# Optimization experiments

Measured on AMD Instinct MI355X. Metric: run time of the kernel, lower is better.

Reference implementation:

```python
import jax, jax.numpy as jnp
import numpy as np

IMAGE_H, IMAGE_W = 256, 704
Z, Y, X = 128, 8, 128
BOUNDS = (-50.0, 50.0, -5.0, 5.0, -50.0, 50.0)
CENTROID = (0.0, 1.0, 0.0)
EPS_MEAN = 1e-6
EPS_DEPTH = 1e-4


def _compose_rt(R, t):
    M = jnp.zeros(R.shape[:-2] + (4, 4), R.dtype)
    M = M.at[..., :3, :3].set(R)
    M = M.at[..., :3, 3].set(t)
    M = M.at[..., 3, 3].set(1.0)
    return M


def _safe_inverse(M):
    R = M[..., :3, :3]
    t = M[..., :3, 3]
    Rt = jnp.swapaxes(R, -1, -2)
    return _compose_rt(Rt, -jnp.einsum('...ij,...j->...i', Rt, t))


def _apply_4x4(M, xyz):
    # M: (...,4,4), xyz: (...,N,3) -> (...,N,3)
    return jnp.einsum('...ij,...nj->...ni', M[..., :3, :3], xyz) + M[..., None, :3, 3]


def _xyz_camA():
    # Mem2Ref of gridcloud3d: x_ref = x_mem*vox + MIN + vox/2 (bounds shifted by centroid)
    xmin = BOUNDS[0] + CENTROID[0]; xmax = BOUNDS[1] + CENTROID[0]
    ymin = BOUNDS[2] + CENTROID[1]; ymax = BOUNDS[3] + CENTROID[1]
    zmin = BOUNDS[4] + CENTROID[2]; zmax = BOUNDS[5] + CENTROID[2]
    vx = (xmax - xmin) / X; vy = (ymax - ymin) / Y; vz = (zmax - zmin) / Z
    zz, yy, xx = jnp.meshgrid(jnp.arange(Z, dtype=jnp.float32),
                              jnp.arange(Y, dtype=jnp.float32),
                              jnp.arange(X, dtype=jnp.float32), indexing='ij')
    x = xx * vx + xmin + vx / 2.0
    y = yy * vy + ymin + vy / 2.0
    z = zz * vz + zmin + vz / 2.0
    return jnp.stack([x, y, z], -1).reshape(Z * Y * X, 3)  # mem order (Z,Y,X)


def _bilinear_sample(img, px, py):
    # img: (C,H,W); px,py: (N,) pixel coords; zeros padding (grid_sample align_corners=False)
    C, H, W = img.shape
    x0 = jnp.floor(px); y0 = jnp.floor(py)
    dx = px - x0; dy = py - y0
    x0i = x0.astype(jnp.int32); y0i = y0.astype(jnp.int32)
    flat = img.reshape(C, H * W)

    def gather(yi, xi, w):
        inb = (xi >= 0) & (xi < W) & (yi >= 0) & (yi < H)
        idx = jnp.clip(yi, 0, H - 1) * W + jnp.clip(xi, 0, W - 1)
        return flat[:, idx] * (w * inb.astype(img.dtype))

    return (gather(y0i, x0i, (1 - dx) * (1 - dy))
            + gather(y0i, x0i + 1, dx * (1 - dy))
            + gather(y0i + 1, x0i, (1 - dx) * dy)
            + gather(y0i + 1, x0i + 1, dx * dy))  # (C,N)


def _forward(cam_feat, camera2ego, cam_intrinsic, conv_w):
    B, S, C, Hf, Wf = cam_feat.shape
    # velo_T_cams = merge_rt(camera2ego R, t); cam0_T_camXs = inv(velo_T_cams[:,0]) @ velo_T_cams
    velo_T_cams = _compose_rt(camera2ego[..., :3, :3], camera2ego[..., :3, 3])
    cam0_T_velo = _safe_inverse(velo_T_cams[:, 0])
    cam0_T_camXs = jnp.einsum('bij,bsjk->bsik', cam0_T_velo, velo_T_cams)
    camXs_T_cam0 = _safe_inverse(cam0_T_camXs)
    # scale_intrinsics with sy = Hf/H*0.284, sx = Wf/W*0.44
    sy = Hf / float(IMAGE_H) * 0.284
    sx = Wf / float(IMAGE_W) * 0.44
    fx = cam_intrinsic[..., 0, 0] * sx
    fy = cam_intrinsic[..., 1, 1] * sy
    cx = cam_intrinsic[..., 0, 2] * sx
    cy = cam_intrinsic[..., 1, 2] * sy
    K = jnp.zeros((B, S, 4, 4), cam_feat.dtype)
    K = K.at[..., 0, 0].set(fx).at[..., 1, 1].set(fy)
    K = K.at[..., 0, 2].set(cx).at[..., 1, 2].set(cy)
    K = K.at[..., 2, 2].set(1.0).at[..., 3, 3].set(1.0)
    pixB_T_cam0 = jnp.einsum('bsij,bsjk->bsik', K, camXs_T_cam0)

    xyz = _xyz_camA()  # (N,3), N = Z*Y*X
    xyz_camB = _apply_4x4(camXs_T_cam0, xyz[None, None])  # (B,S,N,3)
    z_cam = xyz_camB[..., 2]
    xyz_pix = _apply_4x4(pixB_T_cam0, xyz[None, None])
    depth = jnp.maximum(xyz_pix[..., 2], EPS_DEPTH)
    x_pix = xyz_pix[..., 0] / depth
    y_pix = xyz_pix[..., 1] / depth
    valid = ((x_pix > -0.5) & (x_pix < Wf - 0.5)
             & (y_pix > -0.5) & (y_pix < Hf - 0.5)
             & (z_cam > 0.0)).astype(cam_feat.dtype)
    # normalize_grid2d (clamp [-2,2]) then grid_sample align_corners=False unnormalize
    gx = jnp.clip(2.0 * x_pix / (Wf - 1) - 1.0, -2.0, 2.0)
    gy = jnp.clip(2.0 * y_pix / (Hf - 1) - 1.0, -2.0, 2.0)
    px = ((gx + 1.0) * Wf - 1.0) / 2.0
    py = ((gy + 1.0) * Hf - 1.0) / 2.0

    feats = cam_feat.reshape(B * S, C, Hf, Wf)
    vals = jax.vmap(_bilinear_sample)(feats, px.reshape(B * S, -1), py.reshape(B * S, -1))
    vals = vals.reshape(B, S, C, -1) * valid[:, :, None, :]  # (B,S,C,N)
    mask = (jnp.abs(vals) > 0).astype(vals.dtype)
    feat_mem = jnp.sum(vals * mask, axis=1) / (EPS_MEAN + jnp.sum(mask, axis=1))  # (B,C,N)
    feat_mem = feat_mem.reshape(B, C, Z, Y, X)

    # BEV compress: permute(0,1,3,2,4) -> (B, C*Y, Z, X), conv3x3 (no bias), InstanceNorm2d, GELU
    feat_bev = jnp.transpose(feat_mem, (0, 1, 3, 2, 4)).reshape(B, C * Y, Z, X)
    out = jax.lax.conv_general_dilated(feat_bev, conv_w, (1, 1), ((1, 1), (1, 1)),
                                       dimension_numbers=('NCHW', 'OIHW', 'NCHW'))
    mu = jnp.mean(out, axis=(2, 3), keepdims=True)
    var = jnp.var(out, axis=(2, 3), keepdims=True)
    out = (out - mu) / jnp.sqrt(var + 1e-5)
    return jax.nn.gelu(out, approximate=False)


def setup_inputs() -> dict:
    key = jax.random.key(0)
    k1, k2, k3 = jax.random.split(key, 3)
    B, S, C, Hf, Wf = 1, 6, 128, 32, 88
    cam_feat = jax.random.normal(k1, (B, S, C, Hf, Wf), jnp.float32)
    # rigid camera2ego: yaw rotations about the y axis + small translations
    yaws = jnp.arange(S, dtype=jnp.float32) * (2.0 * jnp.pi / S)
    c, s = jnp.cos(yaws), jnp.sin(yaws)
    zr, on = jnp.zeros_like(c), jnp.ones_like(c)
    R = jnp.stack([jnp.stack([c, zr, s], -1),
                   jnp.stack([zr, on, zr], -1),
                   jnp.stack([-s, zr, c], -1)], -2)  # (S,3,3)
    t = jax.random.normal(k2, (S, 3), jnp.float32) * 0.5
    cam2ego = jnp.zeros((B, S, 4, 4), jnp.float32)
    cam2ego = cam2ego.at[0, :, :3, :3].set(R).at[0, :, :3, 3].set(t).at[0, :, 3, 3].set(1.0)
    K = jnp.zeros((B, S, 4, 4), jnp.float32)
    K = K.at[..., 0, 0].set(600.0).at[..., 1, 1].set(600.0)
    K = K.at[..., 0, 2].set(352.0).at[..., 1, 2].set(128.0)
    K = K.at[..., 2, 2].set(1.0).at[..., 3, 3].set(1.0)
    conv_w = jax.random.normal(k3, (128, 128 * Y, 3, 3), jnp.float32) / np.sqrt(128 * Y * 9.0).astype(np.float32)
    return {"cam_feat": cam_feat, "camera2ego": cam2ego, "cam_intrinsic": K, "conv_w": conv_w}


def reference(cam_feat, camera2ego, cam_intrinsic, conv_w):
    return _forward(cam_feat, camera2ego, cam_intrinsic, conv_w)
```

## Files before the change

kernel.cpp:

```cpp
#include <hip/hip_runtime.h>
#include <hip/hip_bf16.h>
#include <math.h>

#define HF 32
#define WF 88
#define NCAM 6
#define CC 128
#define ZD 128
#define YD 8
#define XD 128

using f32x4  = __attribute__((ext_vector_type(4))) float;
using bf16x8 = __attribute__((ext_vector_type(8))) short;

#define OFF_P    0ull
#define OFF_W    512ull
#define OFF_CAMT (OFF_W + 2359296ull)
#define OFF_F    (OFF_CAMT + 8650752ull)
#define OFF_CONV (OFF_F + 34611200ull)

__global__ __launch_bounds__(256) void k_pre(const float* __restrict__ feat,
                                             const float* __restrict__ conv_w,
                                             const float* __restrict__ cam2ego,
                                             const float* __restrict__ intr,
                                             __hip_bfloat16* __restrict__ camT,
                                             __hip_bfloat16* __restrict__ wp,
                                             float* __restrict__ P) {
  __shared__ float tile[128 * 89];
  const int b = blockIdx.x;
  const int t = threadIdx.x;
  if (b < 192) {
    const int s = b >> 5;
    const int hrow = b & 31;
    for (int idx = t; idx < 128 * 88; idx += 256) {
      const int c = idx / 88;
      const int w = idx - c * 88;
      tile[c * 89 + w] = feat[((size_t)(s * CC + c) * HF + hrow) * WF + w];
    }
    __syncthreads();
    const int c = t & 127;
    const int wh = t >> 7;
    for (int i = 0; i < 44; i++) {
      const int w = i * 2 + wh;
      camT[((size_t)(s * HF + hrow) * WF + w) * CC + c] =
          __float2bfloat16(tile[c * 89 + w]);
    }
  } else if (b < 704) {
    const int tt = (b - 192) * 256 + t;
    float v[9];
    #pragma unroll
    for (int d = 0; d < 9; d++) v[d] = conv_w[(size_t)tt * 9 + d];
    #pragma unroll
    for (int d = 0; d < 9; d++) wp[(size_t)d * 131072 + tt] = __float2bfloat16(v[d]);
  } else {
    const int s = t;
    if (s >= NCAM) return;
    const float* M0 = cam2ego;
    const float* Ms = cam2ego + s * 16;
    float Rb[9], tb[3];
    for (int i = 0; i < 3; i++)
      for (int j = 0; j < 3; j++) {
        float v = 0.f;
        for (int k = 0; k < 3; k++) v += Ms[k * 4 + i] * M0[k * 4 + j];
        Rb[i * 3 + j] = v;
      }
    for (int i = 0; i < 3; i++) {
      float v = 0.f;
      for (int k = 0; k < 3; k++) v += Ms[k * 4 + i] * (M0[k * 4 + 3] - Ms[k * 4 + 3]);
      tb[i] = v;
    }
    const float* Ks = intr + s * 16;
    const float sx = (float)WF / 704.0f * 0.44f;
    const float sy = (float)HF / 256.0f * 0.284f;
    const float fx = Ks[0] * sx, fy = Ks[5] * sy;
    const float cx = Ks[2] * sx, cy = Ks[6] * sy;
    float* p = P + s * 12;
    for (int j = 0; j < 3; j++) p[j]     = fx * Rb[j]     + cx * Rb[6 + j];
    p[3]  = fx * tb[0] + cx * tb[2];
    for (int j = 0; j < 3; j++) p[4 + j] = fy * Rb[3 + j] + cy * Rb[6 + j];
    p[7]  = fy * tb[1] + cy * tb[2];
    for (int j = 0; j < 3; j++) p[8 + j] = Rb[6 + j];
    p[11] = tb[2];
  }
}

struct Rec { int off[4]; float w[4]; };

__global__ __launch_bounds__(256) void k2_sample(const __hip_bfloat16* __restrict__ camT,
                                                 const float* __restrict__ P,
                                                 __hip_bfloat16* __restrict__ F) {
  const int bz = blockIdx.x / 65;
  const int bxp = blockIdx.x % 65;
  const int t = threadIdx.x;
  const int sub = t >> 7;
  const int u = t & 127;
  const int bx = bxp * 2 + sub;
  const int zi = bz - 1, xi = bx - 1;
  const int cq = (u & 31) << 2;
  const int yq = u >> 5;
  __hip_bfloat16* Fb = F + ((size_t)bz * 130 + bx) * 1024;
  const bool inplay = !(zi < 0 || zi >= ZD || xi < 0 || xi >= XD);

  __shared__ Rec recs[2][48];
  __shared__ unsigned ymask[2][8];
  const int lane = t & 63;
  const int wv = t >> 6;
  bool vflag = false;
  if ((wv == 0 || wv == 2) && lane < 48 && inplay) {
    const int y = lane / 6, s = lane - y * 6;
    const float* pp = P + s * 12;
    const float vx = 100.0f / 128.0f;
    const float xw = xi * vx - 50.0f + vx * 0.5f;
    const float zw = zi * vx - 50.0f + vx * 0.5f;
    const float yw = y * 1.25f - 4.0f + 0.625f;
    const float zc = pp[8] * xw + pp[9] * yw + pp[10] * zw + pp[11];
    const float xp = pp[0] * xw + pp[1] * yw + pp[2] * zw + pp[3];
    const float yp = pp[4] * xw + pp[5] * yw + pp[6] * zw + pp[7];
    const float dep = fmaxf(zc, 1e-4f);
    const float pxf = xp / dep, pyf = yp / dep;
    const bool valid = (pxf > -0.5f && pxf < (float)WF - 0.5f &&
                        pyf > -0.5f && pyf < (float)HF - 0.5f && zc > 0.0f);
    const float px = pxf * ((float)WF / (float)(WF - 1)) - 0.5f;
    const float py = pyf * ((float)HF / (float)(HF - 1)) - 0.5f;
    const float fx0 = floorf(px), fy0 = floorf(py);
    const float ddx = px - fx0, ddy = py - fy0;
    const int x0i = (int)fx0, y0i = (int)fy0;
    const float vf = valid ? 1.0f : 0.0f;
    float ww[4];
    ww[0] = (1.0f - ddx) * (1.0f - ddy) * vf;
    ww[1] = ddx * (1.0f - ddy) * vf;
    ww[2] = (1.0f - ddx) * ddy * vf;
    ww[3] = ddx * ddy * vf;
    const int cxs[4] = {x0i, x0i + 1, x0i, x0i + 1};
    const int cys[4] = {y0i, y0i, y0i + 1, y0i + 1};
    Rec r;
    float wsum = 0.f;
    #pragma unroll
    for (int k = 0; k < 4; k++) {
      const bool inb = ((unsigned)cxs[k] < WF) && ((unsigned)cys[k] < HF);
      const int xc = min(max(cxs[k], 0), WF - 1);
      const int yc = min(max(cys[k], 0), HF - 1);
      r.w[k] = inb ? ww[k] : 0.0f;
      r.off[k] = (s * (HF * WF) + yc * WF + xc) * CC;
      wsum += r.w[k];
    }
    recs[sub][lane] = r;
    vflag = wsum > 0.0f;
  }
  if (wv == 0 || wv == 2) {
    unsigned long long m = __ballot(vflag);
    if (lane < 8) ymask[wv >> 1][lane] = (unsigned)((m >> (6 * lane)) & 63ull);
  }
  __syncthreads();

  if (!inplay) {
    #pragma unroll
    for (int j = 0; j < 4; j++)
      *reinterpret_cast<unsigned*>(Fb + (cq + j) * 8 + yq * 2) = 0u;
    return;
  }

  float num[2][4] = {{0.f, 0.f, 0.f, 0.f}, {0.f, 0.f, 0.f, 0.f}};
  int cnt[2] = {0, 0};
  #pragma unroll
  for (int yi = 0; yi < 2; yi++) {
    const int y = yq * 2 + yi;
    unsigned ms = ymask[sub][y];
    while (ms) {
      const int s = __builtin_ctz(ms);
      ms &= ms - 1;
      const Rec r = recs[sub][y * 6 + s];
      #pragma unroll
      for (int k = 0; k < 4; k++) {
        const ushort4 uv = *reinterpret_cast<const ushort4*>(&camT[r.off[k] + cq]);
        num[yi][0] += r.w[k] * __bfloat162float(*reinterpret_cast<const __hip_bfloat16*>(&uv.x));
        num[yi][1] += r.w[k] * __bfloat162float(*reinterpret_cast<const __hip_bfloat16*>(&uv.y));
        num[yi][2] += r.w[k] * __bfloat162float(*reinterpret_cast<const __hip_bfloat16*>(&uv.z));
        num[yi][3] += r.w[k] * __bfloat162float(*reinterpret_cast<const __hip_bfloat16*>(&uv.w));
      }
      cnt[yi]++;
    }
  }
  const float inv0 = 1.0f / (1e-6f + (float)cnt[0]);
  const float inv1 = 1.0f / (1e-6f + (float)cnt[1]);
  #pragma unroll
  for (int j = 0; j < 4; j++) {
    __hip_bfloat16 o[2];
    o[0] = __float2bfloat16(num[0][j] * inv0);
    o[1] = __float2bfloat16(num[1][j] * inv1);
    *reinterpret_cast<unsigned*>(Fb + (cq + j) * 8 + yq * 2) =
        *reinterpret_cast<const unsigned*>(o);
  }
}

__device__ __forceinline__ void load_lds16(const void* g, void* l) {
  __builtin_amdgcn_global_load_lds(
      (const __attribute__((address_space(1))) unsigned int*)g,
      (__attribute__((address_space(3))) unsigned int*)l, 16, 0, 0);
}

#define K3_NT 72

__global__ __launch_bounds__(512) void k3_gemm(const __hip_bfloat16* __restrict__ F,
                                               const __hip_bfloat16* __restrict__ Wp,
                                               float* __restrict__ out0,
                                               float* __restrict__ out1) {
  const int orig = (blockIdx.x & 7) * 32 + (blockIdx.x >> 3);
  const int z = orig & 127;
  const int h = orig >> 7;
  const int ciH = h << 9;
  const int tid = threadIdx.x;
  const int w = tid >> 6;
  const int l = tid & 63;
  const int kk = w >> 2;
  const int wq = w & 3;
  const int wm = wq >> 1;
  const int wn = wq & 1;
  __shared__ __hip_bfloat16 lds[4][16384];

  f32x4 acc[4][4];
  #pragma unroll
  for (int m = 0; m < 4; m++)
    #pragma unroll
    for (int n = 0; n < 4; n++)
      acc[m][n] = (f32x4){0.f, 0.f, 0.f, 0.f};

  auto stage_A = [&](int kt) {
    const int buf = kt & 3;
    const int d = kt >> 3;
    const int dz = d / 3, dx = d - dz * 3;
    const int ci0 = ciH + ((kt & 7) << 6);
    const int zbase = (z + dz) * 130 + dx;
    #pragma unroll
    for (int i = 0; i < 2; i++) {
      const int n = w * 128 + i * 64 + l;
      const int row = n >> 3;
      const int q = (n & 7) ^ (row & 7);
      const __hip_bfloat16* src = F + ((size_t)(zbase + row) << 10) + ci0 + (q << 3);
      load_lds16(src, &lds[buf][(w * 128 + i * 64) * 8]);
    }
  };
  auto stage_B = [&](int kt) {
    const int buf = kt & 3;
    const int d = kt >> 3;
    const int ci0 = ciH + ((kt & 7) << 6);
    #pragma unroll
    for (int i = 0; i < 2; i++) {
      const int n = w * 128 + i * 64 + l;
      const int co = n >> 3;
      const int q = (n & 7) ^ (co & 7);
      const __hip_bfloat16* src = Wp + ((size_t)d << 17) + ((size_t)co << 10) + ci0 + (q << 3);
      load_lds16(src, &lds[buf][8192 + (w * 128 + i * 64) * 8]);
    }
  };

  const int r16 = l & 15;
  const int hi = l >> 4;
  const int cslot = kk * 4 + hi;

  auto step = [&](int t, bool doStage, int wcode) {
    const int buf = t & 3;
    bf16x8 a[4], b[4];
    #pragma unroll
    for (int m = 0; m < 4; m++) {
      const int r = wm * 64 + m * 16 + r16;
      const int slot = cslot ^ (r & 7);
      a[m] = *reinterpret_cast<const bf16x8*>(&lds[buf][r * 64 + slot * 8]);
    }
    #pragma unroll
    for (int n = 0; n < 2; n++) {
      const int co = wn * 64 + n * 16 + r16;
      const int slot = cslot ^ (co & 7);
      b[n] = *reinterpret_cast<const bf16x8*>(&lds[buf][8192 + co * 64 + slot * 8]);
    }
    if (doStage) stage_A(t + 3);
    __builtin_amdgcn_s_barrier();
    __builtin_amdgcn_s_setprio(1);
    #pragma unroll
    for (int m = 0; m < 4; m++) {
      acc[m][0] = __builtin_amdgcn_mfma_f32_16x16x32_bf16(a[m], b[0], acc[m][0], 0, 0, 0);
      acc[m][1] = __builtin_amdgcn_mfma_f32_16x16x32_bf16(a[m], b[1], acc[m][1], 0, 0, 0);
    }
    __builtin_amdgcn_s_setprio(0);
    __builtin_amdgcn_s_barrier();
    #pragma unroll
    for (int n = 2; n < 4; n++) {
      const int co = wn * 64 + n * 16 + r16;
      const int slot = cslot ^ (co & 7);
      b[n] = *reinterpret_cast<const bf16x8*>(&lds[buf][8192 + co * 64 + slot * 8]);
    }
    if (doStage) stage_B(t + 3);
    __builtin_amdgcn_s_barrier();
    __builtin_amdgcn_s_setprio(1);
    #pragma unroll
    for (int m = 0; m < 4; m++) {
      acc[m][2] = __builtin_amdgcn_mfma_f32_16x16x32_bf16(a[m], b[2], acc[m][2], 0, 0, 0);
      acc[m][3] = __builtin_amdgcn_mfma_f32_16x16x32_bf16(a[m], b[3], acc[m][3], 0, 0, 0);
    }
    __builtin_amdgcn_s_setprio(0);
    if (wcode == 8)      asm volatile("s_waitcnt vmcnt(8)" ::: "memory");
    else if (wcode == 4) asm volatile("s_waitcnt vmcnt(4)" ::: "memory");
    else if (wcode == 0) asm volatile("s_waitcnt vmcnt(0)" ::: "memory");
    __builtin_amdgcn_s_barrier();
  };

  stage_A(0); stage_B(0); stage_A(1); stage_B(1); stage_A(2); stage_B(2);
  asm volatile("s_waitcnt vmcnt(8)" ::: "memory");
  __builtin_amdgcn_s_barrier();

  for (int t = 0; t < K3_NT - 3; ++t) step(t, true, 8);
  step(K3_NT - 3, false, 4);
  step(K3_NT - 2, false, 0);
  step(K3_NT - 1, false, -1);

  float* red = reinterpret_cast<float*>(&lds[0][0]);
  if (kk == 1) {
    float* dst = red + wq * 4096;
    #pragma unroll
    for (int m = 0; m < 4; m++)
      #pragma unroll
      for (int n = 0; n < 4; n++)
        *reinterpret_cast<f32x4*>(&dst[(m * 4 + n) * 256 + l * 4]) = acc[m][n];
  }
  __syncthreads();
  if (kk == 0) {
    const float* srcr = red + wq * 4096;
    float* outP = h ? out1 : out0;
    #pragma unroll
    for (int m = 0; m < 4; m++) {
      const int xr = wm * 64 + m * 16 + hi * 4;
      #pragma unroll
      for (int n = 0; n < 4; n++) {
        f32x4 o = *reinterpret_cast<const f32x4*>(&srcr[(m * 4 + n) * 256 + l * 4]);
        f32x4 r = acc[m][n] + o;
        const int co = wn * 64 + n * 16 + r16;
        *reinterpret_cast<f32x4*>(&outP[((size_t)co << 14) + (z << 7) + xr]) = r;
      }
    }
  }
}

__device__ __forceinline__ float gelu_exact(float x) {
  return 0.5f * x * (1.0f + erff(x * 0.70710678118654752440f));
}

__global__ __launch_bounds__(1024) void k4_ln(const float* __restrict__ c0,
                                              const float* __restrict__ c1,
                                              float* __restrict__ outp) {
  const int co = blockIdx.x;
  const int t = threadIdx.x;
  const float4* p0 = reinterpret_cast<const float4*>(c0 + ((size_t)co << 14));
  const float4* p1 = reinterpret_cast<const float4*>(c1 + ((size_t)co << 14));
  float4 v[4];
  float s = 0.f, s2 = 0.f;
  #pragma unroll
  for (int i = 0; i < 4; i++) {
    float4 a = p0[t + (i << 10)];
    float4 b = p1[t + (i << 10)];
    float4 r;
    r.x = a.x + b.x; r.y = a.y + b.y; r.z = a.z + b.z; r.w = a.w + b.w;
    v[i] = r;
    s  += r.x + r.y + r.z + r.w;
    s2 += r.x * r.x + r.y * r.y + r.z * r.z + r.w * r.w;
  }
  #pragma unroll
  for (int off = 32; off > 0; off >>= 1) {
    s  += __shfl_down(s, off);
    s2 += __shfl_down(s2, off);
  }
  __shared__ float red[32];
  __shared__ float mb[2];
  const int wv = t >> 6, ln = t & 63;
  if (ln == 0) { red[wv] = s; red[wv + 16] = s2; }
  __syncthreads();
  if (t == 0) {
    float S = 0.f, S2 = 0.f;
    #pragma unroll
    for (int i = 0; i < 16; i++) { S += red[i]; S2 += red[i + 16]; }
    float mu = S * (1.0f / 16384.0f);
    float var = S2 * (1.0f / 16384.0f) - mu * mu;
    mb[0] = mu;
    mb[1] = 1.0f / sqrtf(var + 1e-5f);
  }
  __syncthreads();
  const float mu = mb[0], inv = mb[1];
  float4* op = reinterpret_cast<float4*>(outp + ((size_t)co << 14));
  #pragma unroll
  for (int i = 0; i < 4; i++) {
    float4 x = v[i];
    float4 r;
    r.x = gelu_exact((x.x - mu) * inv);
    r.y = gelu_exact((x.y - mu) * inv);
    r.z = gelu_exact((x.z - mu) * inv);
    r.w = gelu_exact((x.w - mu) * inv);
    op[t + (i << 10)] = r;
  }
}

extern "C" void kernel_launch(void* const* d_in, const int* in_sizes, int n_in,
                              void* d_out, int out_size, void* d_ws, size_t ws_size,
                              hipStream_t stream) {
  const float* cam_feat = (const float*)d_in[0];
  const float* cam2ego  = (const float*)d_in[1];
  const float* intr     = (const float*)d_in[2];
  const float* conv_w   = (const float*)d_in[3];
  float* out = (float*)d_out;
  char* ws = (char*)d_ws;

  float*          P     = (float*)(ws + OFF_P);
  __hip_bfloat16* Wp    = (__hip_bfloat16*)(ws + OFF_W);
  __hip_bfloat16* camT  = (__hip_bfloat16*)(ws + OFF_CAMT);
  __hip_bfloat16* F     = (__hip_bfloat16*)(ws + OFF_F);
  float*          conv0 = (float*)(ws + OFF_CONV);
  float*          conv1 = (float*)(ws + OFF_CAMT);

  hipLaunchKernelGGL(k_pre, dim3(705), dim3(256), 0, stream,
                     cam_feat, conv_w, cam2ego, intr, camT, Wp, P);
  hipLaunchKernelGGL(k2_sample, dim3(130 * 65), dim3(256), 0, stream, camT, P, F);
  hipLaunchKernelGGL(k3_gemm, dim3(256), dim3(512), 0, stream, F, Wp, conv0, conv1);
  hipLaunchKernelGGL(k4_ln, dim3(128), dim3(1024), 0, stream, conv0, conv1, out);
}
```

Measured before the change: 104.0 us.

## Store horizontally paired fp16 features and sample with fdot2

The camera feature transpose now writes fp16 pairs of horizontally adjacent pixels (px, px+1) packed per channel. Each bilinear tap pair then comes from one wider load, and the sampler reads two rows per point instead of four taps. The bilinear weights are packed as fp16 pairs and accumulated with the fdot2 instruction, cutting load count and ALU work in the sampling kernel. In exchange the feature buffer roughly doubles in size and needs extra transpose writes, and precision moves from bf16 to fp16 for both features and weights, with special-case handling at the image edges.

New measurement: 100.7 us. 3.1% less time.

```diff
diff --git a/kernel.cpp b/kernel.cpp
--- a/kernel.cpp
+++ b/kernel.cpp
@@ -12,6 +12,20 @@
 
 using f32x4  = __attribute__((ext_vector_type(4))) float;
 using bf16x8 = __attribute__((ext_vector_type(8))) short;
+using h2     = __attribute__((ext_vector_type(2))) _Float16;
+
+#if defined(__has_builtin)
+#if __has_builtin(__builtin_amdgcn_fdot2)
+#define HAVE_FDOT2 1
+#endif
+#endif
+__device__ __forceinline__ float fdot2f(h2 a, h2 b, float c) {
+#ifdef HAVE_FDOT2
+  return __builtin_amdgcn_fdot2(a, b, c, false);
+#else
+  return c + (float)a[0] * (float)b[0] + (float)a[1] * (float)b[1];
+#endif
+}
 
 #define OFF_P    0ull
 #define OFF_W    512ull
@@ -23,7 +37,7 @@
                                              const float* __restrict__ conv_w,
                                              const float* __restrict__ cam2ego,
                                              const float* __restrict__ intr,
-                                             __hip_bfloat16* __restrict__ camT,
+                                             unsigned* __restrict__ camT2,
                                              __hip_bfloat16* __restrict__ wp,
                                              float* __restrict__ P) {
   __shared__ float tile[128 * 89];
@@ -38,12 +52,14 @@
       tile[c * 89 + w] = feat[((size_t)(s * CC + c) * HF + hrow) * WF + w];
     }
     __syncthreads();
-    const int c = t & 127;
-    const int wh = t >> 7;
-    for (int i = 0; i < 44; i++) {
-      const int w = i * 2 + wh;
-      camT[((size_t)(s * HF + hrow) * WF + w) * CC + c] =
-          __float2bfloat16(tile[c * 89 + w]);
+    unsigned* dst = camT2 + (size_t)(s * 32 + hrow) * 87 * 128;
+    for (int idx = t; idx < 87 * 128; idx += 256) {
+      const int px = idx >> 7;
+      const int c = idx & 127;
+      union { _Float16 h[2]; unsigned u; } pr;
+      pr.h[0] = (_Float16)tile[c * 89 + px];
+      pr.h[1] = (_Float16)tile[c * 89 + px + 1];
+      dst[px * 128 + c] = pr.u;
     }
   } else if (b < 704) {
     const int tt = (b - 192) * 256 + t;
@@ -84,9 +100,9 @@
   }
 }
 
-struct Rec { int off[4]; float w[4]; };
-
-__global__ __launch_bounds__(256) void k2_sample(const __hip_bfloat16* __restrict__ camT,
+struct Rec { int offA; int offB; unsigned wA; unsigned wB; };
+
+__global__ __launch_bounds__(256) void k2_sample(const unsigned* __restrict__ camT2,
                                                  const float* __restrict__ P,
                                                  __hip_bfloat16* __restrict__ F) {
   const int bz = blockIdx.x / 65;
@@ -126,26 +142,25 @@
     const float ddx = px - fx0, ddy = py - fy0;
     const int x0i = (int)fx0, y0i = (int)fy0;
     const float vf = valid ? 1.0f : 0.0f;
-    float ww[4];
-    ww[0] = (1.0f - ddx) * (1.0f - ddy) * vf;
-    ww[1] = ddx * (1.0f - ddy) * vf;
-    ww[2] = (1.0f - ddx) * ddy * vf;
-    ww[3] = ddx * ddy * vf;
-    const int cxs[4] = {x0i, x0i + 1, x0i, x0i + 1};
-    const int cys[4] = {y0i, y0i, y0i + 1, y0i + 1};
+    const float wxl = (1.0f - ddx) * vf, wxr = ddx * vf;
+    int pxi; float sl, sr;
+    if (x0i >= 0 && x0i <= 86)      { pxi = x0i; sl = wxl; sr = wxr; }
+    else if (x0i == -1)             { pxi = 0;   sl = wxr; sr = 0.f; }
+    else if (x0i == 87)             { pxi = 86;  sl = 0.f; sr = wxl; }
+    else                            { pxi = 0;   sl = 0.f; sr = 0.f; }
+    const float fA = ((unsigned)y0i < (unsigned)HF) ? (1.0f - ddy) : 0.0f;
+    const float fB = ((unsigned)(y0i + 1) < (unsigned)HF) ? ddy : 0.0f;
+    const int rowA = min(max(y0i, 0), HF - 1);
+    const int rowB = min(max(y0i + 1, 0), HF - 1);
     Rec r;
-    float wsum = 0.f;
-    #pragma unroll
-    for (int k = 0; k < 4; k++) {
-      const bool inb = ((unsigned)cxs[k] < WF) && ((unsigned)cys[k] < HF);
-      const int xc = min(max(cxs[k], 0), WF - 1);
-      const int yc = min(max(cys[k], 0), HF - 1);
-      r.w[k] = inb ? ww[k] : 0.0f;
-      r.off[k] = (s * (HF * WF) + yc * WF + xc) * CC;
-      wsum += r.w[k];
-    }
+    r.offA = ((s * HF + rowA) * 87 + pxi) * 128;
+    r.offB = ((s * HF + rowB) * 87 + pxi) * 128;
+    union { _Float16 h[2]; unsigned u; } wa, wb;
+    wa.h[0] = (_Float16)(sl * fA); wa.h[1] = (_Float16)(sr * fA);
+    wb.h[0] = (_Float16)(sl * fB); wb.h[1] = (_Float16)(sr * fB);
+    r.wA = wa.u; r.wB = wb.u;
     recs[sub][lane] = r;
-    vflag = wsum > 0.0f;
+    vflag = ((sl + sr) * (fA + fB)) > 0.0f;
   }
   if (wv == 0 || wv == 2) {
     unsigned long long m = __ballot(vflag);
@@ -170,14 +185,18 @@
       const int s = __builtin_ctz(ms);
       ms &= ms - 1;
       const Rec r = recs[sub][y * 6 + s];
-      #pragma unroll
-      for (int k = 0; k < 4; k++) {
-        const ushort4 uv = *reinterpret_cast<const ushort4*>(&camT[r.off[k] + cq]);
-        num[yi][0] += r.w[k] * __bfloat162float(*reinterpret_cast<const __hip_bfloat16*>(&uv.x));
-        num[yi][1] += r.w[k] * __bfloat162float(*reinterpret_cast<const __hip_bfloat16*>(&uv.y));
-        num[yi][2] += r.w[k] * __bfloat162float(*reinterpret_cast<const __hip_bfloat16*>(&uv.z));
-        num[yi][3] += r.w[k] * __bfloat162float(*reinterpret_cast<const __hip_bfloat16*>(&uv.w));
-      }
+      const uint4 a4 = *reinterpret_cast<const uint4*>(&camT2[r.offA + cq]);
+      const uint4 b4 = *reinterpret_cast<const uint4*>(&camT2[r.offB + cq]);
+      const h2 wa = __builtin_bit_cast(h2, r.wA);
+      const h2 wb = __builtin_bit_cast(h2, r.wB);
+      num[yi][0] = fdot2f(__builtin_bit_cast(h2, a4.x), wa, num[yi][0]);
+      num[yi][1] = fdot2f(__builtin_bit_cast(h2, a4.y), wa, num[yi][1]);
+      num[yi][2] = fdot2f(__builtin_bit_cast(h2, a4.z), wa, num[yi][2]);
+      num[yi][3] = fdot2f(__builtin_bit_cast(h2, a4.w), wa, num[yi][3]);
+      num[yi][0] = fdot2f(__builtin_bit_cast(h2, b4.x), wb, num[yi][0]);
+      num[yi][1] = fdot2f(__builtin_bit_cast(h2, b4.y), wb, num[yi][1]);
+      num[yi][2] = fdot2f(__builtin_bit_cast(h2, b4.z), wb, num[yi][2]);
+      num[yi][3] = fdot2f(__builtin_bit_cast(h2, b4.w), wb, num[yi][3]);
       cnt[yi]++;
     }
   }
@@ -409,14 +428,14 @@
 
   float*          P     = (float*)(ws + OFF_P);
   __hip_bfloat16* Wp    = (__hip_bfloat16*)(ws + OFF_W);
-  __hip_bfloat16* camT  = (__hip_bfloat16*)(ws + OFF_CAMT);
+  unsigned*       camT2 = (unsigned*)(ws + OFF_CAMT);
   __hip_bfloat16* F     = (__hip_bfloat16*)(ws + OFF_F);
   float*          conv0 = (float*)(ws + OFF_CONV);
   float*          conv1 = (float*)(ws + OFF_CAMT);
 
   hipLaunchKernelGGL(k_pre, dim3(705), dim3(256), 0, stream,
-                     cam_feat, conv_w, cam2ego, intr, camT, Wp, P);
-  hipLaunchKernelGGL(k2_sample, dim3(130 * 65), dim3(256), 0, stream, camT, P, F);
+                     cam_feat, conv_w, cam2ego, intr, camT2, Wp, P);
+  hipLaunchKernelGGL(k2_sample, dim3(130 * 65), dim3(256), 0, stream, camT2, P, F);
   hipLaunchKernelGGL(k3_gemm, dim3(256), dim3(512), 0, stream, F, Wp, conv0, conv1);
   hipLaunchKernelGGL(k4_ln, dim3(128), dim3(1024), 0, stream, conv0, conv1, out);
 }
```
